# Kernel tuning notes

Measured on AMD Instinct MI355X. Metric: run time of the kernel, lower is better.

## Reference

```python
import jax, jax.numpy as jnp
import numpy as np

N = 4096  # scaled-up NBNEUR


def setup_inputs() -> dict:
    key = jax.random.key(0)
    k1, k2, k3, k4, k5 = jax.random.split(key, 5)
    # small scales keep tanh out of saturation, like the 0.01 init in the source
    return {
        "input": jax.random.normal(k1, (1, N), dtype=jnp.float32) * 0.1,
        "yin": jax.random.normal(k2, (1, N), dtype=jnp.float32) * 0.1,
        "hebb": jax.random.normal(k3, (N, N), dtype=jnp.float32) * 0.01,
        "w": jax.random.normal(k4, (N, N), dtype=jnp.float32) * 0.01,
        "alpha": jax.random.normal(k5, (N, N), dtype=jnp.float32) * 0.01,
        "eta": jnp.full((1,), 0.01, dtype=jnp.float32),
    }


def reference(input, yin, hebb, w, alpha, eta):
    # yout = tanh(yin @ (w + alpha * hebb) + input)   -> [1, N]
    yout = jnp.tanh(yin @ (w + alpha * hebb) + input)
    # hebb' = (1 - eta) * hebb + eta * outer(yin, yout)  -> [N, N]
    outer = yin[0][:, None] * yout[0][None, :]
    hebb_new = (1.0 - eta) * hebb + eta * outer
    return yout, hebb_new
```

## Files before the change

kernel.cpp:

```cpp
#include <hip/hip_runtime.h>

#define NN 4096

template <int RPB>
__global__ __launch_bounds__(256, 8) void matvec_partial_kernel(
    const float* __restrict__ yin,
    const float* __restrict__ w,
    const float* __restrict__ alpha,
    const float* __restrict__ hebb,
    float* __restrict__ part)
{
    const int col = blockIdx.x * 1024 + threadIdx.x * 4;
    const int r0  = blockIdx.y * RPB;

    float4 acc = make_float4(0.f, 0.f, 0.f, 0.f);
    #pragma unroll
    for (int b = 0; b < RPB / 2; ++b) {
        const int i0 = r0 + 2 * b;
        const size_t off0 = (size_t)i0 * NN + col;
        const size_t off1 = off0 + NN;
        const float4 w0 = *reinterpret_cast<const float4*>(w + off0);
        const float4 a0 = *reinterpret_cast<const float4*>(alpha + off0);
        const float4 h0 = *reinterpret_cast<const float4*>(hebb + off0);
        const float4 w1 = *reinterpret_cast<const float4*>(w + off1);
        const float4 a1 = *reinterpret_cast<const float4*>(alpha + off1);
        const float4 h1 = *reinterpret_cast<const float4*>(hebb + off1);
        const float y0 = yin[i0];
        const float y1 = yin[i0 + 1];
        acc.x += y0 * (w0.x + a0.x * h0.x) + y1 * (w1.x + a1.x * h1.x);
        acc.y += y0 * (w0.y + a0.y * h0.y) + y1 * (w1.y + a1.y * h1.y);
        acc.z += y0 * (w0.z + a0.z * h0.z) + y1 * (w1.z + a1.z * h1.z);
        acc.w += y0 * (w0.w + a0.w * h0.w) + y1 * (w1.w + a1.w * h1.w);
    }
    *reinterpret_cast<float4*>(part + (size_t)blockIdx.y * NN + col) = acc;
}

__global__ __launch_bounds__(256) void reduce_yout_kernel(
    const float* __restrict__ part,
    const float* __restrict__ input,
    float* __restrict__ yout,
    int rows)
{
    const int tid   = threadIdx.x;
    const int j     = blockIdx.x * 64 + (tid & 63);
    const int slice = tid >> 6;
    const int per   = rows >> 2;

    float s = 0.f;
    #pragma unroll 8
    for (int kk = 0; kk < per; ++kk)
        s += part[(size_t)(slice * per + kk) * NN + j];

    __shared__ float sm[256];
    sm[tid] = s;
    __syncthreads();
    if (tid < 64) {
        float tot = sm[tid] + sm[tid + 64] + sm[tid + 128] + sm[tid + 192];
        yout[j] = tanhf(tot + input[j]);
    }
}

__global__ __launch_bounds__(256, 8) void hebb_update_kernel(
    const float* __restrict__ hebb,
    const float* __restrict__ yin,
    const float* __restrict__ yout,
    const float* __restrict__ eta_p,
    float* __restrict__ hebb_out)
{
    const float eta = eta_p[0];
    const float om  = 1.0f - eta;
    const int tid   = blockIdx.x * 256 + threadIdx.x;
    const int NT    = 2048 * 256;

    const float4 yo = reinterpret_cast<const float4*>(yout)[tid & 1023];

    #pragma unroll
    for (int half = 0; half < 2; ++half) {
        float4 hv[4];
        float  ye[4];
        #pragma unroll
        for (int it = 0; it < 4; ++it) {
            const int g = tid + (half * 4 + it) * NT;
            hv[it] = reinterpret_cast<const float4*>(hebb)[g];
            ye[it] = eta * yin[g >> 10];
        }
        #pragma unroll
        for (int it = 0; it < 4; ++it) {
            const int g = tid + (half * 4 + it) * NT;
            float4 r;
            r.x = om * hv[it].x + ye[it] * yo.x;
            r.y = om * hv[it].y + ye[it] * yo.y;
            r.z = om * hv[it].z + ye[it] * yo.z;
            r.w = om * hv[it].w + ye[it] * yo.w;
            reinterpret_cast<float4*>(hebb_out)[g] = r;
        }
    }
}

extern "C" void kernel_launch(void* const* d_in, const int* in_sizes, int n_in,
                              void* d_out, int out_size, void* d_ws, size_t ws_size,
                              hipStream_t stream) {
    const float* input = (const float*)d_in[0];
    const float* yin   = (const float*)d_in[1];
    const float* hebb  = (const float*)d_in[2];
    const float* w     = (const float*)d_in[3];
    const float* alpha = (const float*)d_in[4];
    const float* eta   = (const float*)d_in[5];

    float* out      = (float*)d_out;
    float* yout     = out;
    float* hebb_out = out + NN;
    float* part     = (float*)d_ws;

    const size_t bytes_1024 = (size_t)1024 * NN * sizeof(float);

    if (ws_size >= bytes_1024) {
        dim3 g1(4, 1024);
        matvec_partial_kernel<4><<<g1, 256, 0, stream>>>(yin, w, alpha, hebb, part);
        reduce_yout_kernel<<<NN / 64, 256, 0, stream>>>(part, input, yout, 1024);
    } else {
        dim3 g1(4, 256);
        matvec_partial_kernel<16><<<g1, 256, 0, stream>>>(yin, w, alpha, hebb, part);
        reduce_yout_kernel<<<NN / 64, 256, 0, stream>>>(part, input, yout, 256);
    }

    hebb_update_kernel<<<2048, 256, 0, stream>>>(hebb, yin, yout, eta, hebb_out);
}
```

Baseline: 249.4 us.

## Split matvec into separate w and alpha*hebb block groups using output as scratch

The matvec is split into two block populations. One group streams only w, 8 rows per block. The other streams alpha and hebb, 4 rows per block. This gives 1536 row-blocks instead of 1024, with more loads in flight per thread. Partials for the alpha*hebb term go into the hebb_out region of the output, which is overwritten later, so the workspace-size fallback goes away. The cost is more partial sums to reduce (512 plus 1024 rows instead of 1024) and a dependency on the output buffer being large enough to serve as scratch.

```diff
diff --git a/kernel.cpp b/kernel.cpp
--- a/kernel.cpp
+++ b/kernel.cpp
@@ -2,54 +2,83 @@
 
 #define NN 4096
 
-template <int RPB>
 __global__ __launch_bounds__(256, 8) void matvec_partial_kernel(
     const float* __restrict__ yin,
     const float* __restrict__ w,
     const float* __restrict__ alpha,
     const float* __restrict__ hebb,
-    float* __restrict__ part)
+    float* __restrict__ part1,
+    float* __restrict__ part2)
 {
     const int col = blockIdx.x * 1024 + threadIdx.x * 4;
-    const int r0  = blockIdx.y * RPB;
+    const int by  = blockIdx.y;
 
     float4 acc = make_float4(0.f, 0.f, 0.f, 0.f);
-    #pragma unroll
-    for (int b = 0; b < RPB / 2; ++b) {
-        const int i0 = r0 + 2 * b;
-        const size_t off0 = (size_t)i0 * NN + col;
-        const size_t off1 = off0 + NN;
-        const float4 w0 = *reinterpret_cast<const float4*>(w + off0);
-        const float4 a0 = *reinterpret_cast<const float4*>(alpha + off0);
-        const float4 h0 = *reinterpret_cast<const float4*>(hebb + off0);
-        const float4 w1 = *reinterpret_cast<const float4*>(w + off1);
-        const float4 a1 = *reinterpret_cast<const float4*>(alpha + off1);
-        const float4 h1 = *reinterpret_cast<const float4*>(hebb + off1);
-        const float y0 = yin[i0];
-        const float y1 = yin[i0 + 1];
-        acc.x += y0 * (w0.x + a0.x * h0.x) + y1 * (w1.x + a1.x * h1.x);
-        acc.y += y0 * (w0.y + a0.y * h0.y) + y1 * (w1.y + a1.y * h1.y);
-        acc.z += y0 * (w0.z + a0.z * h0.z) + y1 * (w1.z + a1.z * h1.z);
-        acc.w += y0 * (w0.w + a0.w * h0.w) + y1 * (w1.w + a1.w * h1.w);
+
+    if (by < 512) {
+        const int r0 = by * 8;
+        #pragma unroll
+        for (int b = 0; b < 2; ++b) {
+            float4 wv[4];
+            float  yv[4];
+            #pragma unroll
+            for (int k = 0; k < 4; ++k) {
+                const int i = r0 + b * 4 + k;
+                wv[k] = *reinterpret_cast<const float4*>(w + (size_t)i * NN + col);
+                yv[k] = yin[i];
+            }
+            #pragma unroll
+            for (int k = 0; k < 4; ++k) {
+                acc.x += yv[k] * wv[k].x;
+                acc.y += yv[k] * wv[k].y;
+                acc.z += yv[k] * wv[k].z;
+                acc.w += yv[k] * wv[k].w;
+            }
+        }
+        *reinterpret_cast<float4*>(part1 + (size_t)by * NN + col) = acc;
+    } else {
+        const int r0 = (by - 512) * 4;
+        #pragma unroll
+        for (int b = 0; b < 2; ++b) {
+            float4 av[2], hv[2];
+            float  yv[2];
+            #pragma unroll
+            for (int k = 0; k < 2; ++k) {
+                const int i = r0 + b * 2 + k;
+                const size_t off = (size_t)i * NN + col;
+                av[k] = *reinterpret_cast<const float4*>(alpha + off);
+                hv[k] = *reinterpret_cast<const float4*>(hebb + off);
+                yv[k] = yin[i];
+            }
+            #pragma unroll
+            for (int k = 0; k < 2; ++k) {
+                acc.x += yv[k] * (av[k].x * hv[k].x);
+                acc.y += yv[k] * (av[k].y * hv[k].y);
+                acc.z += yv[k] * (av[k].z * hv[k].z);
+                acc.w += yv[k] * (av[k].w * hv[k].w);
+            }
+        }
+        *reinterpret_cast<float4*>(part2 + (size_t)(by - 512) * NN + col) = acc;
     }
-    *reinterpret_cast<float4*>(part + (size_t)blockIdx.y * NN + col) = acc;
 }
 
 __global__ __launch_bounds__(256) void reduce_yout_kernel(
-    const float* __restrict__ part,
+    const float* __restrict__ part1,
+    const float* __restrict__ part2,
     const float* __restrict__ input,
-    float* __restrict__ yout,
-    int rows)
+    float* __restrict__ yout)
 {
     const int tid   = threadIdx.x;
     const int j     = blockIdx.x * 64 + (tid & 63);
     const int slice = tid >> 6;
-    const int per   = rows >> 2;
 
     float s = 0.f;
     #pragma unroll 8
-    for (int kk = 0; kk < per; ++kk)
-        s += part[(size_t)(slice * per + kk) * NN + j];
+    for (int kk = 0; kk < 128; ++kk)
+        s += part1[(size_t)(slice * 128 + kk) * NN + j];
+    #pragma unroll 8
+    for (int kk = 0; kk < 256; ++kk)
+        s += part2[(size_t)(slice * 256 + kk) * NN + j];
 
     __shared__ float sm[256];
     sm[tid] = s;
@@ -110,19 +139,15 @@
     float* out      = (float*)d_out;
     float* yout     = out;
     float* hebb_out = out + NN;
-    float* part     = (float*)d_ws;
 
-    const size_t bytes_1024 = (size_t)1024 * NN * sizeof(float);
+    float* part1 = (float*)d_ws;
+    float* part2 = hebb_out;
 
-    if (ws_size >= bytes_1024) {
-        dim3 g1(4, 1024);
-        matvec_partial_kernel<4><<<g1, 256, 0, stream>>>(yin, w, alpha, hebb, part);
-        reduce_yout_kernel<<<NN / 64, 256, 0, stream>>>(part, input, yout, 1024);
-    } else {
-        dim3 g1(4, 256);
-        matvec_partial_kernel<16><<<g1, 256, 0, stream>>>(yin, w, alpha, hebb, part);
-        reduce_yout_kernel<<<NN / 64, 256, 0, stream>>>(part, input, yout, 256);
-    }
+    dim3 g1(4, 1536);
+    matvec_partial_kernel<<<g1, 256, 0, stream>>>(yin, w, alpha, hebb,
+                                                  part1, part2);
+
+    reduce_yout_kernel<<<NN / 64, 256, 0, stream>>>(part1, part2, input, yout);
 
     hebb_update_kernel<<<2048, 256, 0, stream>>>(hebb, yin, yout, eta, hebb_out);
 }
```

Result: slower. 258.3 us (+3.6%).
